# Optimization experiments

Measured on AMD Instinct MI355X. Metric: run time of the kernel, lower is better.

## Reference

```python
import jax, jax.numpy as jnp
import numpy as np
from jax import lax

B, T_MEL, M = 4, 63, 80
HOP, K_UP, WIN = 256, 800, 1024
R, S, Q = 120, 240, 256
NB, K, CYCLE = 16, 2, 8
PAD_UP = (K_UP + 4 * HOP - WIN) // 2  # 400
L = (T_MEL - 1) * HOP  # 15872


def conv1d(x, w, b, dilation=1, pad=(0, 0)):
    # x: [B,Cin,L], w: [Cout,Cin,K]
    y = lax.conv_general_dilated(x, w, (1,), [pad], rhs_dilation=(dilation,),
                                 dimension_numbers=('NCH', 'OIH', 'NCH'))
    return y + b[None, :, None]


def setup_inputs() -> dict:
    key = jax.random.key(0)
    ks = jax.random.split(key, 20)
    rn = lambda k, shape, s=0.05: (jax.random.normal(k, shape, jnp.float32) * s)
    return {
        'waveforms': jax.random.normal(ks[0], (B, L), jnp.float32),
        'melspecs': jax.random.normal(ks[1], (B, M, T_MEL), jnp.float32),
        # ConvTranspose1d weight, torch layout (in, out, k)
        'w_up': rn(ks[2], (M, M, K_UP)), 'b_up': rn(ks[3], (M,)),
        'w_in': rn(ks[4], (R, 1, 1)), 'b_in': rn(ks[5], (R,)),
        # per-block params stacked on leading axis
        'w_gate': rn(ks[6], (NB, 2 * R, R, K)), 'b_gate': rn(ks[7], (NB, 2 * R)),
        'w_cond': rn(ks[8], (NB, 2 * R, M, 1)), 'b_cond': rn(ks[9], (NB, 2 * R)),
        'w_res': rn(ks[10], (NB, R, R, 1)), 'b_res': rn(ks[11], (NB, R)),
        'w_skip': rn(ks[12], (NB, S, R, 1)), 'b_skip': rn(ks[13], (NB, S)),
        'w_h1': rn(ks[14], (Q, S, 1)), 'b_h1': rn(ks[15], (Q,)),
        'w_h2': rn(ks[16], (Q, Q, 1)), 'b_h2': rn(ks[17], (Q,)),
    }


def reference(waveforms, melspecs, w_up, b_up, w_in, b_in, w_gate, b_gate,
              w_cond, b_cond, w_res, b_res, w_skip, b_skip, w_h1, b_h1, w_h2, b_h2):
    # upsample = ConvTranspose1d: lhs-dilated conv with flipped, transposed kernel
    wt = jnp.flip(jnp.transpose(w_up, (1, 0, 2)), -1)  # [out,in,k]
    p = K_UP - 1 - PAD_UP  # 399
    conditions = lax.conv_general_dilated(
        melspecs, wt, (1,), [(p, p)], lhs_dilation=(HOP,),
        dimension_numbers=('NCH', 'OIH', 'NCH')) + b_up[None, :, None]

    length = min(waveforms.shape[-1], conditions.shape[-1])
    wav = waveforms[..., :length]
    cond = conditions[..., :length]

    residuals = conv1d(wav[:, None, :], w_in, b_in)  # [B,R,L]
    skips = jnp.zeros((wav.shape[0], S, length), residuals.dtype)
    for i in range(NB):
        d = 2 ** (i % CYCLE)
        gated = conv1d(residuals, w_gate[i], b_gate[i], dilation=d, pad=((K - 1) * d, 0))
        gated = gated + conv1d(cond, w_cond[i], b_cond[i])
        f, g = jnp.split(gated, 2, axis=1)
        z = jnp.tanh(f) * jax.nn.sigmoid(g)  # [B,R,L]
        skips = skips + conv1d(z, w_skip[i], b_skip[i])
        residuals = residuals + conv1d(z, w_res[i], b_res[i])

    h = conv1d(jax.nn.relu(skips), w_h1, b_h1)
    logits = conv1d(jax.nn.relu(h), w_h2, b_h2)  # [B,Q,L]
    return logits
```

## Files before the change

### kernel.cpp

```cpp
#include <hip/hip_runtime.h>
#include <math.h>

#define B_   4
#define M_   80
#define TMEL 63
#define R_   120
#define S_   240
#define Q_   256
#define NB_  16
#define L_   15872

typedef float  f32x4  __attribute__((ext_vector_type(4)));
typedef short  bf16x8 __attribute__((ext_vector_type(8)));
typedef short  short4_t __attribute__((ext_vector_type(4)));

__device__ __forceinline__ short f2bf(float x) {
  unsigned u = __builtin_bit_cast(unsigned, x);
  u += 0x7fffu + ((u >> 16) & 1u);
  return (short)(u >> 16);
}
__device__ __forceinline__ float bf2f(unsigned short s) {
  unsigned u = ((unsigned)s) << 16;
  return __builtin_bit_cast(float, u);
}

__global__ __launch_bounds__(256) void prep_melT_kernel(
    const float* __restrict__ mel, short* __restrict__ melT)
{
  const int idx = blockIdx.x * 256 + threadIdx.x;
  if (idx >= B_ * TMEL * M_) return;
  const int m = idx % M_;
  const int i = (idx / M_) % TMEL;
  const int b = idx / (M_ * TMEL);
  melT[idx] = f2bf(mel[b * (M_ * TMEL) + m * TMEL + i]);
}

__global__ __launch_bounds__(256) void prep_wup_kernel(
    const float* __restrict__ w_up, short* __restrict__ Wup)
{
  __shared__ float T[M_][65];
  const int c  = blockIdx.x >> 4;
  const int j  = (blockIdx.x >> 2) & 3;
  const int fb = blockIdx.x & 3;
  for (int idx = threadIdx.x; idx < M_ * 64; idx += 256) {
    const int pl = idx & 63, m = idx >> 6;
    const int phi = fb * 64 + pl;
    const int dmin = (phi < 112) ? -1 : -2;
    const int dmax = (phi < 144) ? 1 : 0;
    const int delta = dmin + j;
    float v = 0.0f;
    if (delta <= dmax)
      v = w_up[m * (M_ * 800) + c * 800 + (400 + phi + 256 * delta)];
    T[m][pl] = v;
  }
  __syncthreads();
  for (int idx = threadIdx.x; idx < 64 * M_; idx += 256) {
    const int m = idx % M_, pl = idx / M_;
    const int phi = fb * 64 + pl;
    Wup[((size_t)phi * M_ + c) * 320 + j * 80 + m] = f2bf(T[m][pl]);
  }
}

#define KPU 328

__global__ __launch_bounds__(256, 2) void upsample_mfma_kernel(
    const short* __restrict__ melT, const short* __restrict__ Wup,
    const float* __restrict__ b_up, short* __restrict__ condb)
{
  __shared__ __align__(16) short Xu[64 * KPU];
  const int tid = threadIdx.x;
  const int phi = blockIdx.x;
  const int r0 = blockIdx.y * 64;
  const int dmin = (phi < 112) ? -1 : -2;

  for (int idx = tid; idx < 2560; idx += 256) {
    const int v = idx % 10;
    const int j = (idx / 10) & 3;
    const int rl = idx / 40;
    const int rho = r0 + rl;
    const int b = rho / 62;
    const int n = rho - b * 62;
    const int i = n - (dmin + j);
    int4 val = make_int4(0, 0, 0, 0);
    if (b < B_ && i >= 0 && i < TMEL)
      val = *(const int4*)&melT[((size_t)b * TMEL + i) * M_ + v * 8];
    *(int4*)&Xu[rl * KPU + j * 80 + v * 8] = val;
  }
  __syncthreads();

  const int lane = tid & 63;
  const int wv = tid >> 6;
  const int col = lane & 15;
  const int quad = lane >> 4;
  const int kq = quad * 8;

  f32x4 acc[5];
#pragma unroll
  for (int i = 0; i < 5; ++i) acc[i] = (f32x4)(0.f);
#pragma unroll
  for (int ks = 0; ks < 10; ++ks) {
    bf16x8 a = *(const bf16x8*)&Xu[(wv * 16 + col) * KPU + ks * 32 + kq];
#pragma unroll
    for (int ct = 0; ct < 5; ++ct) {
      bf16x8 b = *(const bf16x8*)(Wup + ((size_t)phi * M_ + ct * 16 + col) * 320 + ks * 32 + kq);
      acc[ct] = __builtin_amdgcn_mfma_f32_16x16x32_bf16(a, b, acc[ct], 0, 0, 0);
    }
  }
#pragma unroll
  for (int ct = 0; ct < 5; ++ct) {
    const int c = ct * 16 + col;
    const float bc = b_up[c];
#pragma unroll
    for (int reg = 0; reg < 4; ++reg) {
      const int rho = r0 + wv * 16 + quad * 4 + reg;
      if (rho < 248) {
        const int b = rho / 62;
        const int n = rho - b * 62;
        const int t = phi + (n << 8);
        condb[((size_t)b * L_ + t) * M_ + c] = f2bf(acc[ct][reg] + bc);
      }
    }
  }
}

__global__ __launch_bounds__(256) void in_conv_kernel(
    const float* __restrict__ wav, const float* __restrict__ w_in,
    const float* __restrict__ b_in, float* __restrict__ res)
{
  const int idx = blockIdx.x * 256 + threadIdx.x;
  const int r = idx & 127;
  const int rem = idx >> 7;
  const int t = rem % L_;
  const int b = rem / L_;
  res[idx] = (r < R_) ? (w_in[r] * wav[b * L_ + t] + b_in[r]) : 0.0f;
}

__global__ __launch_bounds__(256) void prepack_w1_kernel(
    const float* __restrict__ wg, const float* __restrict__ wc,
    short* __restrict__ W1p)
{
  const int idx = blockIdx.x * 256 + threadIdx.x;
  const int k = idx % 320;
  const int cp = (idx / 320) % 256;
  const int i = idx / (320 * 256);
  float val = 0.0f;
  if (cp < 240) {
    const int r = cp >> 1;
    const int corig = (cp & 1) ? (120 + r) : r;
    if (k < 120)      val = wg[((size_t)(i * 240 + corig) * 120 + k) * 2 + 0];
    else if (k < 240) val = wg[((size_t)(i * 240 + corig) * 120 + (k - 120)) * 2 + 1];
    else              val = wc[(size_t)(i * 240 + corig) * 80 + (k - 240)];
  }
  W1p[idx] = f2bf(val);
}

__global__ __launch_bounds__(256) void prepack_w2_kernel(
    const float* __restrict__ wsk, const float* __restrict__ wr,
    short* __restrict__ W2p)
{
  const int idx = blockIdx.x * 256 + threadIdx.x;
  const int k = idx % 128;
  const int sp = (idx / 128) % 384;
  const int i = idx / (128 * 384);
  float val = 0.0f;
  if (k < 120) {
    if (sp < 240)      val = wsk[(size_t)(i * 240 + sp) * 120 + k];
    else if (sp < 360) val = wr[(size_t)(i * 120 + (sp - 240)) * 120 + k];
  }
  W2p[idx] = f2bf(val);
}

__global__ __launch_bounds__(256) void prepack_rest_kernel(
    const float* __restrict__ wh1, const float* __restrict__ wh2,
    const float* __restrict__ bg, const float* __restrict__ bc,
    const float* __restrict__ bs, const float* __restrict__ br,
    short* __restrict__ Wh1p, short* __restrict__ Wh2p,
    float* __restrict__ bias1p, float* __restrict__ bias2p)
{
  const int idx = blockIdx.x * 256 + threadIdx.x;
  if (idx < 65536) {
    const int q = idx >> 8, k = idx & 255;
    Wh1p[idx] = f2bf(k < 240 ? wh1[q * 240 + k] : 0.0f);
  } else if (idx < 131072) {
    Wh2p[idx - 65536] = f2bf(wh2[idx - 65536]);
  } else if (idx < 134912) {
    const int j = idx - 131072;
    const int i = j / 240, cp = j % 240;
    const int r = cp >> 1;
    const int corig = (cp & 1) ? (120 + r) : r;
    bias1p[j] = bg[i * 240 + corig] + bc[i * 240 + corig];
  } else if (idx < 141056) {
    const int j = idx - 134912;
    const int i = j / 384, sp = j % 384;
    float v = 0.0f;
    if (sp < 240)      v = bs[i * 240 + sp];
    else if (sp < 360) v = br[i * 120 + (sp - 240)];
    bias2p[j] = v;
  }
}

#define KP1 328
#define KP2 136
#define SGP 248

__global__ __launch_bounds__(512, 4) void block_mfma_kernel(
    const float* __restrict__ res_in, float* __restrict__ res_out,
    unsigned short* __restrict__ skips, const short* __restrict__ condb,
    const short* __restrict__ W1, const short* __restrict__ W2,
    const float* __restrict__ bias1, const float* __restrict__ bias2,
    const int d, const int first)
{
  __shared__ __align__(16) short Xs[64 * KP1];
  __shared__ __align__(16) short Zs[64 * KP2];

  const int tid = threadIdx.x;
  const int bb = blockIdx.y;
  const int t0 = blockIdx.x * 64;

  {
    const int dd = (d <= 64) ? d : 64;
    const int nr = 64 + dd;
    for (int idx = tid; idx < nr * 30; idx += 512) {
      const int rr = idx / 30, c4 = idx - rr * 30;
      int ts;
      if (d <= 64)      ts = t0 - d + rr;
      else              ts = (rr < 64) ? (t0 - 128 + rr) : (t0 + rr - 64);
      float4 v = make_float4(0.f, 0.f, 0.f, 0.f);
      if (ts >= 0)
        v = *(const float4*)(res_in + ((size_t)(bb * L_ + ts) * 128 + c4 * 4));
      short4_t s;
      s.x = f2bf(v.x); s.y = f2bf(v.y); s.z = f2bf(v.z); s.w = f2bf(v.w);
      if (rr < 64)
        *(short4_t*)&Xs[rr * KP1 + c4 * 4] = s;
      const int r1 = rr - dd;
      if (r1 >= 0)
        *(short4_t*)&Xs[r1 * KP1 + 120 + c4 * 4] = s;
    }
  }
  for (int idx = tid; idx < 640; idx += 512) {
    const int c = idx % 10, trw = idx / 10;
    const int4 v = *(const int4*)(condb + ((size_t)(bb * L_ + t0 + trw) * M_ + c * 8));
    *(int4*)&Xs[trw * KP1 + 240 + c * 8] = v;
  }
  __syncthreads();

  const int lane = tid & 63;
  const int wv = tid >> 6;
  const int col = lane & 15;
  const int quad = lane >> 4;
  const int kq = quad * 8;

  f32x4 acc[4][2];
#pragma unroll
  for (int a = 0; a < 4; ++a)
#pragma unroll
    for (int b = 0; b < 2; ++b) acc[a][b] = (f32x4)(0.f);
#pragma unroll
  for (int ks = 0; ks < 10; ++ks) {
    bf16x8 av[4];
#pragma unroll
    for (int tf = 0; tf < 4; ++tf)
      av[tf] = *(const bf16x8*)&Xs[(tf * 16 + col) * KP1 + ks * 32 + kq];
#pragma unroll
    for (int ct = 0; ct < 2; ++ct) {
      bf16x8 b = *(const bf16x8*)(W1 + ((wv * 2 + ct) * 16 + col) * 320 + ks * 32 + kq);
#pragma unroll
      for (int tf = 0; tf < 4; ++tf)
        acc[tf][ct] = __builtin_amdgcn_mfma_f32_16x16x32_bf16(av[tf], b, acc[tf][ct], 0, 0, 0);
    }
  }

#pragma unroll
  for (int ct = 0; ct < 2; ++ct) {
    const int tile = wv * 2 + ct;
    if (tile < 15) {
      const int cp = tile * 16 + col;
      const float bias = bias1[cp];
#pragma unroll
      for (int tf = 0; tf < 4; ++tf) {
#pragma unroll
        for (int reg = 0; reg < 4; ++reg) {
          float v = acc[tf][ct][reg] + bias;
          v = fminf(fmaxf(v, -15.f), 15.f);
          const float e = __expf((lane & 1) ? -v : 2.0f * v);
          const float rc = __builtin_amdgcn_rcpf(e + 1.0f);
          const float u = (lane & 1) ? rc : (e - 1.0f) * rc;
          const float p = __shfl_xor(u, 1, 64);
          if (!(lane & 1)) {
            const int t = tf * 16 + quad * 4 + reg;
            Zs[t * KP2 + tile * 8 + (col >> 1)] = f2bf(u * p);
          }
        }
      }
    }
  }
  if (tid < 64)
    *(int4*)&Zs[tid * KP2 + 120] = make_int4(0, 0, 0, 0);
  __syncthreads();

  f32x4 acc2[4][3];
#pragma unroll
  for (int a = 0; a < 4; ++a)
#pragma unroll
    for (int b = 0; b < 3; ++b) acc2[a][b] = (f32x4)(0.f);
#pragma unroll
  for (int ks = 0; ks < 4; ++ks) {
    bf16x8 av[4];
#pragma unroll
    for (int tf = 0; tf < 4; ++tf)
      av[tf] = *(const bf16x8*)&Zs[(tf * 16 + col) * KP2 + ks * 32 + kq];
#pragma unroll
    for (int st = 0; st < 3; ++st) {
      bf16x8 b = *(const bf16x8*)(W2 + ((wv * 3 + st) * 16 + col) * 128 + ks * 32 + kq);
#pragma unroll
      for (int tf = 0; tf < 4; ++tf)
        acc2[tf][st] = __builtin_amdgcn_mfma_f32_16x16x32_bf16(av[tf], b, acc2[tf][st], 0, 0, 0);
    }
  }

  short* SG = Xs;
#pragma unroll
  for (int st = 0; st < 3; ++st) {
    const int tile = wv * 3 + st;
    if (tile < 15) {
      const int s = tile * 16 + col;
      const float b2 = bias2[s];
#pragma unroll
      for (int tf = 0; tf < 4; ++tf)
#pragma unroll
        for (int reg = 0; reg < 4; ++reg)
          SG[(tf * 16 + quad * 4 + reg) * SGP + s] = f2bf(acc2[tf][st][reg] + b2);
    } else if (tile < 23) {
      const int s = tile * 16 + col;
      const int r = s - 240;
      if (r < 120) {
        const float b2 = bias2[s];
#pragma unroll
        for (int tf = 0; tf < 4; ++tf) {
#pragma unroll
          for (int reg = 0; reg < 4; ++reg) {
            const int t = tf * 16 + quad * 4 + reg;
            const size_t gi = ((size_t)(bb * L_ + t0 + t)) * 128 + r;
            res_out[gi] = res_in[gi] + acc2[tf][st][reg] + b2;
          }
        }
      }
    }
  }
  __syncthreads();

  {
    const size_t srow = ((size_t)bb * L_ + t0) * 240;
#pragma unroll
    for (int it = 0; it < 4; ++it) {
      const int idx = tid + it * 512;
      if (idx < 1920) {
        const int row = idx / 30;
        const int j = idx - row * 30;
        unsigned short* gp = skips + srow + row * 240 + j * 8;
        int4 sv = *(const int4*)&SG[row * SGP + j * 8];
        const unsigned short* svp = (const unsigned short*)&sv;
        float vals[8];
#pragma unroll
        for (int e = 0; e < 8; ++e) vals[e] = bf2f(svp[e]);
        if (!first) {
          int4 ov = *(const int4*)gp;
          const unsigned short* ovp = (const unsigned short*)&ov;
#pragma unroll
          for (int e = 0; e < 8; ++e) vals[e] += bf2f(ovp[e]);
        }
        int4 res;
        unsigned short* rp = (unsigned short*)&res;
#pragma unroll
        for (int e = 0; e < 8; ++e) rp[e] = (unsigned short)f2bf(vals[e]);
        *(int4*)gp = res;
      }
    }
  }
}

#define KPH 264

__global__ __launch_bounds__(256, 2) void head_mfma_kernel(
    const unsigned short* __restrict__ skips,
    const short* __restrict__ Wh1, const short* __restrict__ Wh2,
    const float* __restrict__ bh1, const float* __restrict__ bh2,
    float* __restrict__ out)
{
  __shared__ __align__(16) short Ss[64 * KPH];
  __shared__ __align__(16) short Hs[64 * KPH];

  const int tid = threadIdx.x;
  const int bb = blockIdx.y;
  const int t0 = blockIdx.x * 64;

  for (int idx = tid; idx < 2048; idx += 256) {
    const int c = idx & 31, trw = idx >> 5;
    if (c < 30) {
      int4 v = *(const int4*)(skips + ((size_t)(bb * L_ + t0 + trw) * 240 + c * 8));
      int* vi = (int*)&v;
#pragma unroll
      for (int j = 0; j < 4; ++j) {
        unsigned x = (unsigned)vi[j];
        unsigned lo = x & 0xFFFFu; if (lo & 0x8000u) lo = 0;
        unsigned hi = x >> 16;     if (hi & 0x8000u) hi = 0;
        vi[j] = (int)(lo | (hi << 16));
      }
      *(int4*)&Ss[trw * KPH + c * 8] = v;
    } else {
      *(int4*)&Ss[trw * KPH + c * 8] = make_int4(0, 0, 0, 0);
    }
  }
  __syncthreads();

  const int lane = tid & 63;
  const int wv = tid >> 6;
  const int col = lane & 15;
  const int quad = lane >> 4;
  const int kq = quad * 8;

  f32x4 acc[4][4];
#pragma unroll
  for (int a = 0; a < 4; ++a)
#pragma unroll
    for (int b = 0; b < 4; ++b) acc[a][b] = (f32x4)(0.f);
#pragma unroll
  for (int ks = 0; ks < 8; ++ks) {
    bf16x8 av[4];
#pragma unroll
    for (int tf = 0; tf < 4; ++tf)
      av[tf] = *(const bf16x8*)&Ss[(tf * 16 + col) * KPH + ks * 32 + kq];
#pragma unroll
    for (int ct = 0; ct < 4; ++ct) {
      bf16x8 b = *(const bf16x8*)(Wh1 + ((wv * 4 + ct) * 16 + col) * 256 + ks * 32 + kq);
#pragma unroll
      for (int tf = 0; tf < 4; ++tf)
        acc[tf][ct] = __builtin_amdgcn_mfma_f32_16x16x32_bf16(av[tf], b, acc[tf][ct], 0, 0, 0);
    }
  }
#pragma unroll
  for (int ct = 0; ct < 4; ++ct) {
    const int q = (wv * 4 + ct) * 16 + col;
    const float b1 = bh1[q];
#pragma unroll
    for (int tf = 0; tf < 4; ++tf)
#pragma unroll
      for (int reg = 0; reg < 4; ++reg)
        Hs[(tf * 16 + quad * 4 + reg) * KPH + q] = f2bf(fmaxf(acc[tf][ct][reg] + b1, 0.0f));
  }
  __syncthreads();

  f32x4 acc2[4][4];
#pragma unroll
  for (int a = 0; a < 4; ++a)
#pragma unroll
    for (int b = 0; b < 4; ++b) acc2[a][b] = (f32x4)(0.f);
#pragma unroll
  for (int ks = 0; ks < 8; ++ks) {
    bf16x8 av[4];
#pragma unroll
    for (int tf = 0; tf < 4; ++tf)
      av[tf] = *(const bf16x8*)&Hs[(tf * 16 + col) * KPH + ks * 32 + kq];
#pragma unroll
    for (int ct = 0; ct < 4; ++ct) {
      bf16x8 b = *(const bf16x8*)(Wh2 + ((wv * 4 + ct) * 16 + col) * 256 + ks * 32 + kq);
#pragma unroll
      for (int tf = 0; tf < 4; ++tf)
        acc2[tf][ct] = __builtin_amdgcn_mfma_f32_16x16x32_bf16(av[tf], b, acc2[tf][ct], 0, 0, 0);
    }
  }
#pragma unroll
  for (int ct = 0; ct < 4; ++ct) {
    const int q = (wv * 4 + ct) * 16 + col;
    const float b2 = bh2[q];
#pragma unroll
    for (int tf = 0; tf < 4; ++tf) {
      const int tg0 = t0 + tf * 16 + quad * 4;
      float4 o = make_float4(acc2[tf][ct][0] + b2, acc2[tf][ct][1] + b2,
                             acc2[tf][ct][2] + b2, acc2[tf][ct][3] + b2);
      *(float4*)(out + ((size_t)(bb * Q_ + q)) * L_ + tg0) = o;
    }
  }
}

extern "C" void kernel_launch(void* const* d_in, const int* in_sizes, int n_in,
                              void* d_out, int out_size, void* d_ws, size_t ws_size,
                              hipStream_t stream) {
  const float* wav    = (const float*)d_in[0];
  const float* mel    = (const float*)d_in[1];
  const float* w_up   = (const float*)d_in[2];
  const float* b_up   = (const float*)d_in[3];
  const float* w_in   = (const float*)d_in[4];
  const float* b_in   = (const float*)d_in[5];
  const float* w_gate = (const float*)d_in[6];
  const float* b_gate = (const float*)d_in[7];
  const float* w_cond = (const float*)d_in[8];
  const float* b_cond = (const float*)d_in[9];
  const float* w_res  = (const float*)d_in[10];
  const float* b_res  = (const float*)d_in[11];
  const float* w_skip = (const float*)d_in[12];
  const float* b_skip = (const float*)d_in[13];
  const float* w_h1   = (const float*)d_in[14];
  const float* b_h1   = (const float*)d_in[15];
  const float* w_h2   = (const float*)d_in[16];
  const float* b_h2   = (const float*)d_in[17];
  float* out = (float*)d_out;

  char* w = (char*)d_ws;
  short* condb   = (short*)w;                 w += (size_t)B_ * L_ * M_ * 2;
  float* res0    = (float*)w;                 w += (size_t)B_ * L_ * 128 * 4;
  float* res1    = (float*)w;                 w += (size_t)B_ * L_ * 128 * 4;
  unsigned short* skips = (unsigned short*)w; w += (size_t)B_ * L_ * 240 * 2;
  short* W1p     = (short*)w;                 w += (size_t)16 * 256 * 320 * 2;
  short* W2p     = (short*)w;                 w += (size_t)16 * 384 * 128 * 2;
  short* Wh1p    = (short*)w;                 w += (size_t)256 * 256 * 2;
  short* Wh2p    = (short*)w;                 w += (size_t)256 * 256 * 2;
  float* bias1p  = (float*)w;                 w += (size_t)16 * 240 * 4;
  float* bias2p  = (float*)w;                 w += (size_t)16 * 384 * 4;
  short* melT    = (short*)w;                 w += (size_t)B_ * TMEL * M_ * 2;
  short* Wup = (short*)skips;

  prepack_w1_kernel<<<(16 * 256 * 320) / 256, 256, 0, stream>>>(w_gate, w_cond, W1p);
  prepack_w2_kernel<<<(16 * 384 * 128) / 256, 256, 0, stream>>>(w_skip, w_res, W2p);
  prepack_rest_kernel<<<141056 / 256, 256, 0, stream>>>(
      w_h1, w_h2, b_gate, b_cond, b_skip, b_res, Wh1p, Wh2p, bias1p, bias2p);
  prep_melT_kernel<<<(B_ * TMEL * M_ + 255) / 256, 256, 0, stream>>>(mel, melT);
  prep_wup_kernel<<<80 * 4 * 4, 256, 0, stream>>>(w_up, Wup);

  dim3 ugrid(256, 4);
  upsample_mfma_kernel<<<ugrid, 256, 0, stream>>>(melT, Wup, b_up, condb);
  in_conv_kernel<<<((size_t)B_ * L_ * 128) / 256, 256, 0, stream>>>(wav, w_in, b_in, res0);

  dim3 bgrid(L_ / 64, B_);
  for (int i = 0; i < NB_; ++i) {
    const int d = 1 << (i & 7);
    const float* rin  = (i & 1) ? res1 : res0;
    float*       rout = (i & 1) ? res0 : res1;
    block_mfma_kernel<<<bgrid, 512, 0, stream>>>(
        rin, rout, skips, condb,
        W1p + (size_t)i * 256 * 320, W2p + (size_t)i * 384 * 128,
        bias1p + i * 240, bias2p + i * 384,
        d, (i == 0) ? 1 : 0);
  }

  head_mfma_kernel<<<bgrid, 256, 0, stream>>>(skips, Wh1p, Wh2p, b_h1, b_h2, out);
}
```

Before: 1.109 ms.

## Alias Z and skip staging into one LDS buffer and simplify bf16 rounding

Removes the separate Zs shared buffer and stores the gated activations at an offset inside Xs, adding barriers so the overwrite is safe. This cuts LDS per block so the launch bound can rise from 4 to 6 blocks per CU. The bf16 conversion drops round-to-nearest-even for a plain add-0x8000, and pairs of values are packed with a perm instruction. In exchange there are two extra __syncthreads, higher register pressure from holding zv, and slightly different rounding on ties.

```diff
diff --git a/kernel.cpp b/kernel.cpp
--- a/kernel.cpp
+++ b/kernel.cpp
@@ -15,9 +15,13 @@
 typedef short  short4_t __attribute__((ext_vector_type(4)));
 
 __device__ __forceinline__ short f2bf(float x) {
-  unsigned u = __builtin_bit_cast(unsigned, x);
-  u += 0x7fffu + ((u >> 16) & 1u);
+  unsigned u = __builtin_bit_cast(unsigned, x) + 0x8000u;
   return (short)(u >> 16);
+}
+__device__ __forceinline__ unsigned bfpack(float hi, float lo) {
+  unsigned a = __builtin_bit_cast(unsigned, hi) + 0x8000u;
+  unsigned b = __builtin_bit_cast(unsigned, lo) + 0x8000u;
+  return __builtin_amdgcn_perm(a, b, 0x07060302u);
 }
 __device__ __forceinline__ float bf2f(unsigned short s) {
   unsigned u = ((unsigned)s) << 16;
@@ -200,10 +204,9 @@
 }
 
 #define KP1 328
-#define KP2 136
-#define SGP 248
-
-__global__ __launch_bounds__(512, 4) void block_mfma_kernel(
+#define ZOFF 184
+
+__global__ __launch_bounds__(512, 6) void block_mfma_kernel(
     const float* __restrict__ res_in, float* __restrict__ res_out,
     unsigned short* __restrict__ skips, const short* __restrict__ condb,
     const short* __restrict__ W1, const short* __restrict__ W2,
@@ -211,7 +214,6 @@
     const int d, const int first)
 {
   __shared__ __align__(16) short Xs[64 * KP1];
-  __shared__ __align__(16) short Zs[64 * KP2];
 
   const int tid = threadIdx.x;
   const int bb = blockIdx.y;
@@ -228,13 +230,14 @@
       float4 v = make_float4(0.f, 0.f, 0.f, 0.f);
       if (ts >= 0)
         v = *(const float4*)(res_in + ((size_t)(bb * L_ + ts) * 128 + c4 * 4));
-      short4_t s;
-      s.x = f2bf(v.x); s.y = f2bf(v.y); s.z = f2bf(v.z); s.w = f2bf(v.w);
+      uint2 p;
+      p.x = bfpack(v.y, v.x);
+      p.y = bfpack(v.w, v.z);
       if (rr < 64)
-        *(short4_t*)&Xs[rr * KP1 + c4 * 4] = s;
+        *(uint2*)&Xs[rr * KP1 + c4 * 4] = p;
       const int r1 = rr - dd;
       if (r1 >= 0)
-        *(short4_t*)&Xs[r1 * KP1 + 120 + c4 * 4] = s;
+        *(uint2*)&Xs[r1 * KP1 + 120 + c4 * 4] = p;
     }
   }
   for (int idx = tid; idx < 640; idx += 512) {
@@ -270,12 +273,12 @@
     }
   }
 
+  float zv[2][4][4];
 #pragma unroll
   for (int ct = 0; ct < 2; ++ct) {
     const int tile = wv * 2 + ct;
     if (tile < 15) {
-      const int cp = tile * 16 + col;
-      const float bias = bias1[cp];
+      const float bias = bias1[tile * 16 + col];
 #pragma unroll
       for (int tf = 0; tf < 4; ++tf) {
 #pragma unroll
@@ -286,16 +289,29 @@
           const float rc = __builtin_amdgcn_rcpf(e + 1.0f);
           const float u = (lane & 1) ? rc : (e - 1.0f) * rc;
           const float p = __shfl_xor(u, 1, 64);
+          zv[ct][tf][reg] = u * p;
+        }
+      }
+    }
+  }
+  __syncthreads();
+
+#pragma unroll
+  for (int ct = 0; ct < 2; ++ct) {
+    const int tile = wv * 2 + ct;
+    if (tile < 15) {
+#pragma unroll
+      for (int tf = 0; tf < 4; ++tf)
+#pragma unroll
+        for (int reg = 0; reg < 4; ++reg)
           if (!(lane & 1)) {
             const int t = tf * 16 + quad * 4 + reg;
-            Zs[t * KP2 + tile * 8 + (col >> 1)] = f2bf(u * p);
+            Xs[t * KP1 + ZOFF + tile * 8 + (col >> 1)] = f2bf(zv[ct][tf][reg]);
           }
-        }
-      }
     }
   }
   if (tid < 64)
-    *(int4*)&Zs[tid * KP2 + 120] = make_int4(0, 0, 0, 0);
+    *(int4*)&Xs[tid * KP1 + ZOFF + 120] = make_int4(0, 0, 0, 0);
   __syncthreads();
 
   f32x4 acc2[4][3];
@@ -308,7 +324,7 @@
     bf16x8 av[4];
 #pragma unroll
     for (int tf = 0; tf < 4; ++tf)
-      av[tf] = *(const bf16x8*)&Zs[(tf * 16 + col) * KP2 + ks * 32 + kq];
+      av[tf] = *(const bf16x8*)&Xs[(tf * 16 + col) * KP1 + ZOFF + ks * 32 + kq];
 #pragma unroll
     for (int st = 0; st < 3; ++st) {
       bf16x8 b = *(const bf16x8*)(W2 + ((wv * 3 + st) * 16 + col) * 128 + ks * 32 + kq);
@@ -317,8 +333,8 @@
         acc2[tf][st] = __builtin_amdgcn_mfma_f32_16x16x32_bf16(av[tf], b, acc2[tf][st], 0, 0, 0);
     }
   }
-
-  short* SG = Xs;
+  __syncthreads();
+
 #pragma unroll
   for (int st = 0; st < 3; ++st) {
     const int tile = wv * 3 + st;
@@ -329,7 +345,7 @@
       for (int tf = 0; tf < 4; ++tf)
 #pragma unroll
         for (int reg = 0; reg < 4; ++reg)
-          SG[(tf * 16 + quad * 4 + reg) * SGP + s] = f2bf(acc2[tf][st][reg] + b2);
+          Xs[(tf * 16 + quad * 4 + reg) * KP1 + s] = f2bf(acc2[tf][st][reg] + b2);
     } else if (tile < 23) {
       const int s = tile * 16 + col;
       const int r = s - 240;
@@ -358,7 +374,7 @@
         const int row = idx / 30;
         const int j = idx - row * 30;
         unsigned short* gp = skips + srow + row * 240 + j * 8;
-        int4 sv = *(const int4*)&SG[row * SGP + j * 8];
+        int4 sv = *(const int4*)&Xs[row * KP1 + j * 8];
         const unsigned short* svp = (const unsigned short*)&sv;
         float vals[8];
 #pragma unroll
@@ -370,9 +386,10 @@
           for (int e = 0; e < 8; ++e) vals[e] += bf2f(ovp[e]);
         }
         int4 res;
-        unsigned short* rp = (unsigned short*)&res;
-#pragma unroll
-        for (int e = 0; e < 8; ++e) rp[e] = (unsigned short)f2bf(vals[e]);
+        unsigned* rp = (unsigned*)&res;
+#pragma unroll
+        for (int e = 0; e < 4; ++e)
+          rp[e] = bfpack(vals[2 * e + 1], vals[2 * e]);
         *(int4*)gp = res;
       }
     }
```

Measured after the change: 1.607 ms. +44.9%, slower.
